# Kernel tuning notes

Hardware: AMD Instinct MI355X
Metric: run time of the kernel (lower is better)

Reference implementation:

```python
import jax, jax.numpy as jnp
import numpy as np
import math

B, T, N_EMBD, HEAD_SIZE = 8, 2048, 768, 128


def setup_inputs() -> dict:
    key = jax.random.key(0)
    ks = jax.random.split(key, 7)
    s = 0.02
    return {
        "x": jax.random.normal(ks[0], (B, T, N_EMBD), dtype=jnp.float32),
        "Wq": jax.random.normal(ks[1], (N_EMBD, HEAD_SIZE), dtype=jnp.float32) * s,
        "bq": jax.random.normal(ks[2], (HEAD_SIZE,), dtype=jnp.float32) * s,
        "Wk": jax.random.normal(ks[3], (N_EMBD, HEAD_SIZE), dtype=jnp.float32) * s,
        "bk": jax.random.normal(ks[4], (HEAD_SIZE,), dtype=jnp.float32) * s,
        "Wv": jax.random.normal(ks[5], (N_EMBD, HEAD_SIZE), dtype=jnp.float32) * s,
        "bv": jax.random.normal(ks[6], (HEAD_SIZE,), dtype=jnp.float32) * s,
    }


def reference(x, Wq, bq, Wk, bk, Wv, bv):
    # x: [B, T, n_embd]
    Tlen = x.shape[1]
    q = x @ Wq + bq  # [B, T, hs]
    k = x @ Wk + bk
    v = x @ Wv + bv
    scores = jnp.einsum('bqd,bkd->bqk', q, k)  # [B, T, T]
    causal = jnp.tril(jnp.ones((Tlen, Tlen), dtype=bool))
    # original masks with -inf first, then divides by sqrt(head_size); -inf/scale == -inf,
    # so mask-then-scale is mathematically identical.
    scores = jnp.where(causal, scores, -jnp.inf) / math.sqrt(q.shape[-1])
    weights = jax.nn.softmax(scores, axis=-1)
    # dropout p=0.0 (inference/reference) -> identity
    out = jnp.einsum('bqk,bkd->bqd', weights, v)  # [B, T, hs]
    return out
```

## Files before the change

kernel.cpp:

```cpp
#include <hip/hip_runtime.h>

#define B_ 8
#define T_ 2048
#define E_ 768
#define D_ 128
#define SCALE 0.08838834764831845f

typedef _Float16 h8 __attribute__((ext_vector_type(8)));
typedef _Float16 h4 __attribute__((ext_vector_type(4)));
typedef float f4 __attribute__((ext_vector_type(4)));

typedef __attribute__((address_space(1))) unsigned int as1_u32;
typedef __attribute__((address_space(3))) unsigned int as3_u32;

__device__ __forceinline__ void gl_lds16(const void* g, void* l) {
    __builtin_amdgcn_global_load_lds((const as1_u32*)g, (as3_u32*)l, 16, 0, 0);
}

__global__ __launch_bounds__(256) void w_prep(
    const float* __restrict__ Wq, const float* __restrict__ Wk,
    const float* __restrict__ Wv, _Float16* __restrict__ Wh)
{
    __shared__ float tile[64][129];
    const int y = blockIdx.x / 12, kc = blockIdx.x % 12;
    const float* W = (y == 0) ? Wq : (y == 1) ? Wk : Wv;
    const int k0 = kc * 64, t = threadIdx.x;
#pragma unroll
    for (int i = 0; i < 32; ++i) {
        const int idx = i * 256 + t;
        tile[idx >> 7][idx & 127] = W[(size_t)(k0 + (idx >> 7)) * D_ + (idx & 127)];
    }
    __syncthreads();
    const int n = t >> 1, hf = t & 1;
#pragma unroll
    for (int j = 0; j < 4; ++j) {
        const int kk = hf * 32 + j * 8;
        h8 hv;
#pragma unroll
        for (int e = 0; e < 8; ++e) hv[e] = (_Float16)tile[kk + e][n];
        *(h8*)&Wh[(size_t)(y * 128 + n) * E_ + k0 + kk] = hv;
    }
}

__global__ __launch_bounds__(256) void qkv_fused(
    const float* __restrict__ x, const _Float16* __restrict__ Wh,
    const float* __restrict__ bq, const float* __restrict__ bk,
    const float* __restrict__ bv,
    _Float16* __restrict__ Qh, _Float16* __restrict__ Kh,
    _Float16* __restrict__ Vt)
{
    __shared__ _Float16 As[2][64 * 64];
    __shared__ _Float16 Bs[2][384 * 64];

    const int t = threadIdx.x;
    const int lane = t & 63, w = t >> 6;
    const int quad = lane >> 4, col = lane & 15;
    const int m0 = blockIdx.x * 64;

    f4 acc[4][6];
#pragma unroll
    for (int mt = 0; mt < 4; ++mt)
#pragma unroll
        for (int nt = 0; nt < 6; ++nt) acc[mt][nt] = (f4){0.f, 0.f, 0.f, 0.f};

    const int brl = lane >> 3, bc = lane & 7;
    const int xr_ = t >> 2, xcb = (t & 3) * 16;

    float4 xv[4];

#define LOAD_X(kb)                                                          \
    {   const float* xr = &x[(size_t)(m0 + xr_) * E_ + (kb) + xcb];         \
        _Pragma("unroll")                                                   \
        for (int i = 0; i < 4; ++i) xv[i] = *(const float4*)(xr + 4 * i);   }

#define STAGE_B(dst, kb)                                                    \
    _Pragma("unroll")                                                       \
    for (int i = 0; i < 12; ++i) {                                          \
        const int R = w * 96 + i * 8;                                       \
        const int r = R + brl;                                              \
        gl_lds16(Wh + (size_t)r * E_ + (kb) + 8 * (bc ^ (r & 7)), &(dst)[R * 64]); }

#define WRITE_A(dst)                                                        \
    _Pragma("unroll")                                                       \
    for (int i = 0; i < 4; ++i) {                                           \
        h4 hv; hv[0] = (_Float16)xv[i].x; hv[1] = (_Float16)xv[i].y;        \
        hv[2] = (_Float16)xv[i].z; hv[3] = (_Float16)xv[i].w;               \
        const int kk4 = xcb + 4 * i;                                        \
        *(h4*)&(dst)[xr_ * 64 + (((kk4 >> 3) ^ (xr_ & 7)) << 3) + (kk4 & 7)] = hv; }

    LOAD_X(0);
    STAGE_B(Bs[0], 0);
    asm volatile("s_waitcnt vmcnt(12)" ::: "memory");
    WRITE_A(As[0]);
    __syncthreads();

#pragma unroll 2
    for (int it = 0; it < 12; ++it) {
        const int c = it & 1;
        if (it < 11) {
            LOAD_X((it + 1) * 64);
            STAGE_B(Bs[c ^ 1], (it + 1) * 64);
        }
#pragma unroll
        for (int ks = 0; ks < 2; ++ks) {
            const int sc = ((ks << 2) + quad) ^ (col & 7);
            h8 a[4], bf[6];
#pragma unroll
            for (int mt = 0; mt < 4; ++mt)
                a[mt] = *(const h8*)&As[c][(mt * 16 + col) * 64 + (sc << 3)];
#pragma unroll
            for (int nt = 0; nt < 6; ++nt)
                bf[nt] = *(const h8*)&Bs[c][(w * 96 + nt * 16 + col) * 64 + (sc << 3)];
#pragma unroll
            for (int mt = 0; mt < 4; ++mt)
#pragma unroll
                for (int nt = 0; nt < 6; ++nt)
                    acc[mt][nt] = __builtin_amdgcn_mfma_f32_16x16x32_f16(
                        a[mt], bf[nt], acc[mt][nt], 0, 0, 0);
        }
        if (it < 11) {
            asm volatile("s_waitcnt vmcnt(12)" ::: "memory");
            WRITE_A(As[c ^ 1]);
        }
        __syncthreads();
    }

    const float* bp[3] = {bq, bk, bv};
    _Float16* Cs = &Bs[0][0];
#pragma unroll
    for (int nt = 0; nt < 6; ++nt) {
        const int n16 = w * 96 + nt * 16;
        const int y = n16 >> 7, nl = n16 & 127;
        const float bb = bp[y][nl + col];
#pragma unroll
        for (int mt = 0; mt < 4; ++mt)
#pragma unroll
            for (int reg = 0; reg < 4; ++reg) {
                const int m = mt * 16 + quad * 4 + reg;
                Cs[m * 384 + n16 + col] = (_Float16)(acc[mt][nt][reg] + bb);
            }
    }
    __syncthreads();

    {
        const int m = t >> 2, seg = t & 3;
#pragma unroll
        for (int j = 0; j < 8; ++j) {
            const int n = seg * 64 + j * 8;
            const h8 v = *(const h8*)&Cs[m * 384 + n];
            if (n < 128) *(h8*)&Qh[(size_t)(m0 + m) * D_ + n] = v;
            else         *(h8*)&Kh[(size_t)(m0 + m) * D_ + (n - 128)] = v;
        }
    }
    {
        const int vn = t & 127, part = t >> 7;
        const int bidx = m0 >> 11, tt0 = m0 & 2047;
#pragma unroll
        for (int j = 0; j < 4; ++j) {
            const int ms = part * 32 + j * 8;
            h8 hv;
#pragma unroll
            for (int e = 0; e < 8; ++e) hv[e] = Cs[(ms + e) * 384 + 256 + vn];
            *(h8*)&Vt[((size_t)bidx * D_ + vn) * T_ + tt0 + ms] = hv;
        }
    }
#undef LOAD_X
#undef STAGE_B
#undef WRITE_A
}

__global__ __launch_bounds__(256, 2) void flash_attn(
    const _Float16* __restrict__ Qh,
    const _Float16* __restrict__ Kh,
    const _Float16* __restrict__ Vt,
    float* __restrict__ out)
{
    __shared__ __align__(16) char smem[70656];
    _Float16* Ks = (_Float16*)smem;
    _Float16* Vs = (_Float16*)(smem + 32768);
    _Float16* Pb = (_Float16*)(smem + 65536);

    const int t = threadIdx.x, lane = t & 63, w = t >> 6;
    const int quad = lane >> 4, col = lane & 15;
    const int id = blockIdx.x;
    const int b = id & 7;
    const int j32 = 63 - (id >> 3);
    const int qw = w & 1, kh = w >> 1;
    const int qbase = j32 * 32;
    const int qrow0 = qbase + qw * 16;
    const int nk = (j32 >> 1) + 1;

    h8 qf[4];
    const _Float16* Qp = Qh + ((size_t)b * T_ + qrow0 + col) * D_ + quad * 8;
#pragma unroll
    for (int ks = 0; ks < 4; ++ks) qf[ks] = *(const h8*)(Qp + ks * 32);
    asm volatile("s_waitcnt vmcnt(0)" ::: "memory");

    f4 o[8];
#pragma unroll
    for (int i = 0; i < 8; ++i) o[i] = (f4){0.f, 0.f, 0.f, 0.f};
    float m_st[4], l_st[4];
#pragma unroll
    for (int r = 0; r < 4; ++r) { m_st[r] = -1e30f; l_st[r] = 0.f; }

    const _Float16* Kb = Kh + (size_t)b * T_ * D_;
    const _Float16* Vb = Vt + (size_t)b * D_ * T_;
    const int krl = lane >> 4, kc = lane & 15;
    const int vrl = lane >> 3, vc = lane & 7;
    const int cx = col & 7;

    auto stage = [&](int buf, int kbase) __attribute__((always_inline)) {
        _Float16* KsB = Ks + buf * 8192;
        _Float16* VsB = Vs + buf * 8192;
#pragma unroll
        for (int i = 0; i < 4; ++i) {
            const int R = w * 16 + i * 4;
            const int r = R + krl;
            gl_lds16(Kb + (size_t)(kbase + r) * D_ + 8 * (kc ^ (r & 7)), KsB + R * D_);
        }
#pragma unroll
        for (int i = 0; i < 4; ++i) {
            const int R = w * 32 + i * 8;
            const int d = R + vrl;
            gl_lds16(Vb + (size_t)d * T_ + kbase + 8 * (vc ^ (d & 7)), VsB + R * 64);
        }
    };

    _Float16* Pw = Pb + w * 640;

    auto step = [&](int ti, int buf, bool mask) __attribute__((always_inline)) {
        const _Float16* KsB = Ks + buf * 8192;
        const _Float16* VsB = Vs + buf * 8192;

        f4 s[2];
        s[0] = (f4){0.f, 0.f, 0.f, 0.f};
        s[1] = (f4){0.f, 0.f, 0.f, 0.f};
        __builtin_amdgcn_s_setprio(1);
#pragma unroll
        for (int nt = 0; nt < 2; ++nt) {
            const int r = kh * 32 + nt * 16 + col;
#pragma unroll
            for (int ks = 0; ks < 4; ++ks) {
                const h8 kf = *(const h8*)(KsB + r * D_ + 8 * (((ks << 2) + quad) ^ cx));
                s[nt] = __builtin_amdgcn_mfma_f32_16x16x32_f16(qf[ks], kf, s[nt], 0, 0, 0);
            }
        }
        __builtin_amdgcn_s_setprio(0);

        if (mask) {
#pragma unroll
            for (int nt = 0; nt < 2; ++nt) {
                const int key = ti * 64 + kh * 32 + nt * 16 + col;
#pragma unroll
                for (int reg = 0; reg < 4; ++reg) {
                    const int qr = qrow0 + quad * 4 + reg;
                    const float sv = s[nt][reg] * SCALE;
                    s[nt][reg] = (key <= qr) ? sv : -1e30f;
                }
            }
        } else {
#pragma unroll
            for (int nt = 0; nt < 2; ++nt)
#pragma unroll
                for (int reg = 0; reg < 4; ++reg) s[nt][reg] *= SCALE;
        }

        float mloc[4];
#pragma unroll
        for (int reg = 0; reg < 4; ++reg) mloc[reg] = fmaxf(s[0][reg], s[1][reg]);
#pragma unroll
        for (int off = 1; off < 16; off <<= 1)
#pragma unroll
            for (int reg = 0; reg < 4; ++reg)
                mloc[reg] = fmaxf(mloc[reg], __shfl_xor(mloc[reg], off));

        bool grow = (mloc[0] > m_st[0]) | (mloc[1] > m_st[1]) |
                    (mloc[2] > m_st[2]) | (mloc[3] > m_st[3]);
        if (__any((int)grow)) {
#pragma unroll
            for (int reg = 0; reg < 4; ++reg) {
                const float mn = fmaxf(m_st[reg], mloc[reg]);
                const float alpha = __expf(m_st[reg] - mn);
                m_st[reg] = mn;
                l_st[reg] *= alpha;
#pragma unroll
                for (int n2 = 0; n2 < 8; ++n2) o[n2][reg] *= alpha;
            }
        }

        float rs[4] = {0.f, 0.f, 0.f, 0.f};
#pragma unroll
        for (int nt = 0; nt < 2; ++nt)
#pragma unroll
            for (int reg = 0; reg < 4; ++reg) {
                const float p = __expf(s[nt][reg] - m_st[reg]);
                s[nt][reg] = p;
                rs[reg] += p;
            }
#pragma unroll
        for (int off = 1; off < 16; off <<= 1)
#pragma unroll
            for (int reg = 0; reg < 4; ++reg) rs[reg] += __shfl_xor(rs[reg], off);
#pragma unroll
        for (int reg = 0; reg < 4; ++reg) l_st[reg] += rs[reg];

#pragma unroll
        for (int nt = 0; nt < 2; ++nt)
#pragma unroll
            for (int reg = 0; reg < 4; ++reg)
                Pw[(quad * 4 + reg) * 40 + nt * 16 + col] = (_Float16)s[nt][reg];
        const h8 pa = *(const h8*)(Pw + col * 40 + quad * 8);

        __builtin_amdgcn_s_setprio(1);
#pragma unroll
        for (int n2 = 0; n2 < 8; ++n2) {
            const int d = n2 * 16 + col;
            const h8 vf = *(const h8*)(VsB + d * 64 + 8 * ((kh * 4 + quad) ^ (d & 7)));
            o[n2] = __builtin_amdgcn_mfma_f32_16x16x32_f16(pa, vf, o[n2], 0, 0, 0);
        }
        __builtin_amdgcn_s_setprio(0);
    };

    stage(0, 0);
    const bool evenJ = ((j32 & 1) == 0);
    for (int ti = 0; ti < nk; ++ti) {
        const int cur = ti & 1;
        if (ti + 1 < nk) {
            stage(cur ^ 1, (ti + 1) << 6);
            asm volatile("s_waitcnt vmcnt(8)" ::: "memory");
        } else {
            asm volatile("s_waitcnt vmcnt(0)" ::: "memory");
        }
        __builtin_amdgcn_s_barrier();
        const bool last = (ti == nk - 1);
        if (!(last && evenJ && kh == 1)) {
            const bool mask = last && (kh == (j32 & 1));
            step(ti, cur, mask);
        }
        __builtin_amdgcn_s_barrier();
    }

    float* Os = (float*)smem;
    float* Mx = (float*)(smem + 16384);
    float* Lx = Mx + 32;

    __syncthreads();
    if (kh == 1) {
#pragma unroll
        for (int reg = 0; reg < 4; ++reg) {
            const int row = qw * 16 + quad * 4 + reg;
            if (col == 0) { Mx[row] = m_st[reg]; Lx[row] = l_st[reg]; }
#pragma unroll
            for (int n2 = 0; n2 < 8; ++n2)
                Os[row * D_ + n2 * 16 + col] = o[n2][reg];
        }
    }
    __syncthreads();
    if (kh == 0) {
#pragma unroll
        for (int reg = 0; reg < 4; ++reg) {
            const int row = qw * 16 + quad * 4 + reg;
            const float m1 = Mx[row], l1 = Lx[row];
            const float mN = fmaxf(m_st[reg], m1);
            const float a0 = __expf(m_st[reg] - mN);
            const float a1 = __expf(m1 - mN);
            const float inv = 1.0f / (l_st[reg] * a0 + l1 * a1);
#pragma unroll
            for (int n2 = 0; n2 < 8; ++n2) {
                const float v = (o[n2][reg] * a0 + Os[row * D_ + n2 * 16 + col] * a1) * inv;
                out[((size_t)b * T_ + qbase + row) * D_ + n2 * 16 + col] = v;
            }
        }
    }
}

extern "C" void kernel_launch(void* const* d_in, const int* in_sizes, int n_in,
                              void* d_out, int out_size, void* d_ws, size_t ws_size,
                              hipStream_t stream) {
    const float* x  = (const float*)d_in[0];
    const float* Wq = (const float*)d_in[1];
    const float* bq = (const float*)d_in[2];
    const float* Wk = (const float*)d_in[3];
    const float* bk = (const float*)d_in[4];
    const float* Wv = (const float*)d_in[5];
    const float* bv = (const float*)d_in[6];

    _Float16* Qh = (_Float16*)d_ws;
    _Float16* Kh = Qh + (size_t)B_ * T_ * D_;
    _Float16* Vt = Kh + (size_t)B_ * T_ * D_;
    _Float16* Wh = (_Float16*)d_out;

    w_prep<<<dim3(36), dim3(256), 0, stream>>>(Wq, Wk, Wv, Wh);
    qkv_fused<<<dim3(B_ * T_ / 64), dim3(256), 0, stream>>>(
        x, Wh, bq, bk, bv, Qh, Kh, Vt);
    flash_attn<<<dim3(512), dim3(256), 0, stream>>>(Qh, Kh, Vt, (float*)d_out);
}
```

Before: 173.4 us.

## Transpose attention MFMAs for per-lane row softmax, exp2, single-buffer QKV staging

The attention kernel swaps the MFMA operand order so each lane holds one query row. The softmax max and sum then need only two cross-lane shuffles instead of sixteen per row, and exponentials use exp2 with log2(e) folded into the scale. The output epilogue stages results through padded LDS and writes coalesced float4 rows. The QKV GEMM drops the double-buffered B tile in favour of one buffer with extra barriers and sets launch_bounds occupancy to 2 to cut LDS use, at the cost of less load/compute overlap in that kernel.

```diff
diff --git a/kernel.cpp b/kernel.cpp
--- a/kernel.cpp
+++ b/kernel.cpp
@@ -4,10 +4,11 @@
 #define T_ 2048
 #define E_ 768
 #define D_ 128
-#define SCALE 0.08838834764831845f
+#define SCALE2 (0.08838834764831845f * 1.4426950408889634f)
 
 typedef _Float16 h8 __attribute__((ext_vector_type(8)));
 typedef _Float16 h4 __attribute__((ext_vector_type(4)));
+typedef _Float16 h2 __attribute__((ext_vector_type(2)));
 typedef float f4 __attribute__((ext_vector_type(4)));
 
 typedef __attribute__((address_space(1))) unsigned int as1_u32;
@@ -42,7 +43,7 @@
     }
 }
 
-__global__ __launch_bounds__(256) void qkv_fused(
+__global__ __launch_bounds__(256, 2) void qkv_fused(
     const float* __restrict__ x, const _Float16* __restrict__ Wh,
     const float* __restrict__ bq, const float* __restrict__ bk,
     const float* __restrict__ bv,
@@ -50,7 +51,7 @@
     _Float16* __restrict__ Vt)
 {
     __shared__ _Float16 As[2][64 * 64];
-    __shared__ _Float16 Bs[2][384 * 64];
+    __shared__ _Float16 Bs[384 * 64];
 
     const int t = threadIdx.x;
     const int lane = t & 63, w = t >> 6;
@@ -73,12 +74,12 @@
         _Pragma("unroll")                                                   \
         for (int i = 0; i < 4; ++i) xv[i] = *(const float4*)(xr + 4 * i);   }
 
-#define STAGE_B(dst, kb)                                                    \
+#define STAGE_B(kb)                                                         \
     _Pragma("unroll")                                                       \
     for (int i = 0; i < 12; ++i) {                                          \
         const int R = w * 96 + i * 8;                                       \
         const int r = R + brl;                                              \
-        gl_lds16(Wh + (size_t)r * E_ + (kb) + 8 * (bc ^ (r & 7)), &(dst)[R * 64]); }
+        gl_lds16(Wh + (size_t)r * E_ + (kb) + 8 * (bc ^ (r & 7)), &Bs[R * 64]); }
 
 #define WRITE_A(dst)                                                        \
     _Pragma("unroll")                                                       \
@@ -89,18 +90,16 @@
         *(h4*)&(dst)[xr_ * 64 + (((kk4 >> 3) ^ (xr_ & 7)) << 3) + (kk4 & 7)] = hv; }
 
     LOAD_X(0);
-    STAGE_B(Bs[0], 0);
+    STAGE_B(0);
     asm volatile("s_waitcnt vmcnt(12)" ::: "memory");
     WRITE_A(As[0]);
-    __syncthreads();
+    LOAD_X(64);
+    asm volatile("s_waitcnt vmcnt(4) lgkmcnt(0)" ::: "memory");
+    __builtin_amdgcn_s_barrier();
 
 #pragma unroll 2
     for (int it = 0; it < 12; ++it) {
         const int c = it & 1;
-        if (it < 11) {
-            LOAD_X((it + 1) * 64);
-            STAGE_B(Bs[c ^ 1], (it + 1) * 64);
-        }
 #pragma unroll
         for (int ks = 0; ks < 2; ++ks) {
             const int sc = ((ks << 2) + quad) ^ (col & 7);
@@ -110,7 +109,7 @@
                 a[mt] = *(const h8*)&As[c][(mt * 16 + col) * 64 + (sc << 3)];
 #pragma unroll
             for (int nt = 0; nt < 6; ++nt)
-                bf[nt] = *(const h8*)&Bs[c][(w * 96 + nt * 16 + col) * 64 + (sc << 3)];
+                bf[nt] = *(const h8*)&Bs[(w * 96 + nt * 16 + col) * 64 + (sc << 3)];
 #pragma unroll
             for (int mt = 0; mt < 4; ++mt)
 #pragma unroll
@@ -119,14 +118,26 @@
                         a[mt], bf[nt], acc[mt][nt], 0, 0, 0);
         }
         if (it < 11) {
-            asm volatile("s_waitcnt vmcnt(12)" ::: "memory");
+            asm volatile("s_waitcnt vmcnt(0)" ::: "memory");
             WRITE_A(As[c ^ 1]);
-        }
-        __syncthreads();
+            asm volatile("s_waitcnt lgkmcnt(0)" ::: "memory");
+            __builtin_amdgcn_s_barrier();
+            STAGE_B((it + 1) * 64);
+            if (it < 10) {
+                LOAD_X((it + 2) * 64);
+                asm volatile("s_waitcnt vmcnt(4)" ::: "memory");
+            } else {
+                asm volatile("s_waitcnt vmcnt(0)" ::: "memory");
+            }
+            __builtin_amdgcn_s_barrier();
+        } else {
+            asm volatile("s_waitcnt vmcnt(0)" ::: "memory");
+            __builtin_amdgcn_s_barrier();
+        }
     }
 
     const float* bp[3] = {bq, bk, bv};
-    _Float16* Cs = &Bs[0][0];
+    _Float16* Cs = &Bs[0];
 #pragma unroll
     for (int nt = 0; nt < 6; ++nt) {
         const int n16 = w * 96 + nt * 16;
@@ -199,9 +210,7 @@
     f4 o[8];
 #pragma unroll
     for (int i = 0; i < 8; ++i) o[i] = (f4){0.f, 0.f, 0.f, 0.f};
-    float m_st[4], l_st[4];
-#pragma unroll
-    for (int r = 0; r < 4; ++r) { m_st[r] = -1e30f; l_st[r] = 0.f; }
+    float m_st = -1e30f, l_st = 0.f;
 
     const _Float16* Kb = Kh + (size_t)b * T_ * D_;
     const _Float16* Vb = Vt + (size_t)b * D_ * T_;
@@ -242,81 +251,71 @@
 #pragma unroll
             for (int ks = 0; ks < 4; ++ks) {
                 const h8 kf = *(const h8*)(KsB + r * D_ + 8 * (((ks << 2) + quad) ^ cx));
-                s[nt] = __builtin_amdgcn_mfma_f32_16x16x32_f16(qf[ks], kf, s[nt], 0, 0, 0);
+                s[nt] = __builtin_amdgcn_mfma_f32_16x16x32_f16(kf, qf[ks], s[nt], 0, 0, 0);
             }
         }
         __builtin_amdgcn_s_setprio(0);
 
+        const int qr = qrow0 + col;
         if (mask) {
 #pragma unroll
             for (int nt = 0; nt < 2; ++nt) {
-                const int key = ti * 64 + kh * 32 + nt * 16 + col;
+                const int key = ti * 64 + kh * 32 + nt * 16 + quad * 4;
 #pragma unroll
                 for (int reg = 0; reg < 4; ++reg) {
-                    const int qr = qrow0 + quad * 4 + reg;
-                    const float sv = s[nt][reg] * SCALE;
-                    s[nt][reg] = (key <= qr) ? sv : -1e30f;
+                    const float sv = s[nt][reg] * SCALE2;
+                    s[nt][reg] = (key + reg <= qr) ? sv : -1e30f;
                 }
             }
         } else {
 #pragma unroll
             for (int nt = 0; nt < 2; ++nt)
 #pragma unroll
-                for (int reg = 0; reg < 4; ++reg) s[nt][reg] *= SCALE;
-        }
-
-        float mloc[4];
-#pragma unroll
-        for (int reg = 0; reg < 4; ++reg) mloc[reg] = fmaxf(s[0][reg], s[1][reg]);
-#pragma unroll
-        for (int off = 1; off < 16; off <<= 1)
-#pragma unroll
-            for (int reg = 0; reg < 4; ++reg)
-                mloc[reg] = fmaxf(mloc[reg], __shfl_xor(mloc[reg], off));
-
-        bool grow = (mloc[0] > m_st[0]) | (mloc[1] > m_st[1]) |
-                    (mloc[2] > m_st[2]) | (mloc[3] > m_st[3]);
-        if (__any((int)grow)) {
+                for (int reg = 0; reg < 4; ++reg) s[nt][reg] *= SCALE2;
+        }
+
+        float mloc = fmaxf(fmaxf(fmaxf(s[0][0], s[0][1]), fmaxf(s[0][2], s[0][3])),
+                           fmaxf(fmaxf(s[1][0], s[1][1]), fmaxf(s[1][2], s[1][3])));
+        mloc = fmaxf(mloc, __shfl_xor(mloc, 16));
+        mloc = fmaxf(mloc, __shfl_xor(mloc, 32));
+
+        if (__any((int)(mloc > m_st))) {
+            const float mn = fmaxf(m_st, mloc);
+            const float al = __builtin_amdgcn_exp2f(m_st - mn);
+            m_st = mn;
+            l_st *= al;
+#pragma unroll
+            for (int n2 = 0; n2 < 8; ++n2) o[n2] *= al;
+        }
+
+        float rs = 0.f;
+#pragma unroll
+        for (int nt = 0; nt < 2; ++nt)
 #pragma unroll
             for (int reg = 0; reg < 4; ++reg) {
-                const float mn = fmaxf(m_st[reg], mloc[reg]);
-                const float alpha = __expf(m_st[reg] - mn);
-                m_st[reg] = mn;
-                l_st[reg] *= alpha;
-#pragma unroll
-                for (int n2 = 0; n2 < 8; ++n2) o[n2][reg] *= alpha;
-            }
-        }
-
-        float rs[4] = {0.f, 0.f, 0.f, 0.f};
-#pragma unroll
-        for (int nt = 0; nt < 2; ++nt)
-#pragma unroll
-            for (int reg = 0; reg < 4; ++reg) {
-                const float p = __expf(s[nt][reg] - m_st[reg]);
+                const float p = __builtin_amdgcn_exp2f(s[nt][reg] - m_st);
                 s[nt][reg] = p;
-                rs[reg] += p;
-            }
-#pragma unroll
-        for (int off = 1; off < 16; off <<= 1)
-#pragma unroll
-            for (int reg = 0; reg < 4; ++reg) rs[reg] += __shfl_xor(rs[reg], off);
-#pragma unroll
-        for (int reg = 0; reg < 4; ++reg) l_st[reg] += rs[reg];
-
-#pragma unroll
-        for (int nt = 0; nt < 2; ++nt)
-#pragma unroll
-            for (int reg = 0; reg < 4; ++reg)
-                Pw[(quad * 4 + reg) * 40 + nt * 16 + col] = (_Float16)s[nt][reg];
-        const h8 pa = *(const h8*)(Pw + col * 40 + quad * 8);
+                rs += p;
+            }
+        rs += __shfl_xor(rs, 16);
+        rs += __shfl_xor(rs, 32);
+        l_st += rs;
+
+#pragma unroll
+        for (int nt = 0; nt < 2; ++nt) {
+            h2 p0; p0[0] = (_Float16)s[nt][0]; p0[1] = (_Float16)s[nt][1];
+            h2 p1; p1[0] = (_Float16)s[nt][2]; p1[1] = (_Float16)s[nt][3];
+            *(h2*)&Pw[col * 40 + nt * 16 + quad * 4]     = p0;
+            *(h2*)&Pw[col * 40 + nt * 16 + quad * 4 + 2] = p1;
+        }
+        const h8 pa = *(const h8*)&Pw[col * 40 + quad * 8];
 
         __builtin_amdgcn_s_setprio(1);
 #pragma unroll
         for (int n2 = 0; n2 < 8; ++n2) {
             const int d = n2 * 16 + col;
             const h8 vf = *(const h8*)(VsB + d * 64 + 8 * ((kh * 4 + quad) ^ (d & 7)));
-            o[n2] = __builtin_amdgcn_mfma_f32_16x16x32_f16(pa, vf, o[n2], 0, 0, 0);
+            o[n2] = __builtin_amdgcn_mfma_f32_16x16x32_f16(vf, pa, o[n2], 0, 0, 0);
         }
         __builtin_amdgcn_s_setprio(0);
     };
@@ -341,36 +340,41 @@
     }
 
     float* Os = (float*)smem;
-    float* Mx = (float*)(smem + 16384);
+    float* Mx = (float*)(smem + 16896);
     float* Lx = Mx + 32;
+    const int qloc = qw * 16 + col;
 
     __syncthreads();
     if (kh == 1) {
-#pragma unroll
-        for (int reg = 0; reg < 4; ++reg) {
-            const int row = qw * 16 + quad * 4 + reg;
-            if (col == 0) { Mx[row] = m_st[reg]; Lx[row] = l_st[reg]; }
-#pragma unroll
-            for (int n2 = 0; n2 < 8; ++n2)
-                Os[row * D_ + n2 * 16 + col] = o[n2][reg];
-        }
+        if (quad == 0) { Mx[qloc] = m_st; Lx[qloc] = l_st; }
+#pragma unroll
+        for (int n2 = 0; n2 < 8; ++n2)
+#pragma unroll
+            for (int reg = 0; reg < 4; ++reg)
+                Os[qloc * 132 + n2 * 16 + quad * 4 + reg] = o[n2][reg];
     }
     __syncthreads();
     if (kh == 0) {
-#pragma unroll
-        for (int reg = 0; reg < 4; ++reg) {
-            const int row = qw * 16 + quad * 4 + reg;
-            const float m1 = Mx[row], l1 = Lx[row];
-            const float mN = fmaxf(m_st[reg], m1);
-            const float a0 = __expf(m_st[reg] - mN);
-            const float a1 = __expf(m1 - mN);
-            const float inv = 1.0f / (l_st[reg] * a0 + l1 * a1);
-#pragma unroll
-            for (int n2 = 0; n2 < 8; ++n2) {
-                const float v = (o[n2][reg] * a0 + Os[row * D_ + n2 * 16 + col] * a1) * inv;
-                out[((size_t)b * T_ + qbase + row) * D_ + n2 * 16 + col] = v;
-            }
-        }
+        const float m1 = Mx[qloc], l1 = Lx[qloc];
+        const float mN = fmaxf(m_st, m1);
+        const float a0 = __builtin_amdgcn_exp2f(m_st - mN);
+        const float a1 = __builtin_amdgcn_exp2f(m1 - mN);
+        const float inv = 1.0f / (l_st * a0 + l1 * a1);
+#pragma unroll
+        for (int n2 = 0; n2 < 8; ++n2)
+#pragma unroll
+            for (int reg = 0; reg < 4; ++reg) {
+                const int d = n2 * 16 + quad * 4 + reg;
+                Os[qloc * 132 + d] = (o[n2][reg] * a0 + Os[qloc * 132 + d] * a1) * inv;
+            }
+    }
+    __syncthreads();
+    {
+        const int row = t >> 3, d0 = (t & 7) * 16;
+        float* op = &out[((size_t)b * T_ + qbase + row) * D_ + d0];
+#pragma unroll
+        for (int j = 0; j < 4; ++j)
+            *(float4*)(op + j * 4) = *(const float4*)&Os[row * 132 + d0 + j * 4];
     }
 }
 
```

New measurement: 163.1 us. 5.9% less time.
